# Performance work log

Hardware: AMD Instinct MI355X
Metric: run time of the kernel (lower is better)

Reference implementation:

```python
import jax, jax.numpy as jnp
from jax import lax
import numpy as np

CLASS_NUMBER = 19
REGION_RADIUS = 1
KERNEL = 2 * REGION_RADIUS + 1  # 3
IMAGE_TOPK = 256
EPS = 1e-6


def setup_inputs() -> dict:
    key = jax.random.key(0)
    # softmax-like probabilities over classes
    raw = jax.random.uniform(key, (4, CLASS_NUMBER, 512, 1024), dtype=jnp.float32)
    logit = raw / jnp.sum(raw, axis=1, keepdims=True)
    return {"logit": logit}


def _box_sum(x):
    # kxk box sum with zero padding (SAME for odd kernel == pad=radius)
    return lax.reduce_window(x, jnp.float32(0), lax.add,
                             (1, 1, KERNEL, KERNEL), (1, 1, 1, 1), 'SAME')


def reference(logit):
    B, C, H, W = logit.shape
    logC = jnp.log(jnp.float32(C))

    # region uncertainty: normalized entropy, then avg-pool (count_include_pad)
    entropy = jnp.sum(-logit * jnp.log(logit + EPS), axis=1, keepdims=True) / logC
    region_uncertainty = _box_sum(entropy) / (KERNEL * KERNEL)  # [B,1,H,W]

    # region impurity: argmax -> one-hot -> depthwise box-sum (ones kernel)
    predict = jnp.argmax(logit, axis=1)                       # [B,H,W]
    one_hot = jax.nn.one_hot(predict, C, axis=1, dtype=logit.dtype)  # [B,C,H,W]
    summary = _box_sum(one_hot)                               # [B,C,H,W]
    count = jnp.sum(summary, axis=1, keepdims=True)           # [B,1,H,W]
    dist = summary / count
    region_impurity = jnp.sum(-dist * jnp.log(dist + EPS), axis=1, keepdims=True) / logC

    score = region_uncertainty * region_impurity              # [B,1,H,W]

    # per-image score: sum of top-k region scores
    flat = score.reshape(B, H * W)
    topk_vals, _ = lax.top_k(flat, IMAGE_TOPK)
    image_score = jnp.sum(topk_vals, axis=1)                  # [B]
    return image_score
```

## Files before the change

### kernel.cpp

```cpp
#include <hip/hip_runtime.h>
#include <cstdint>
#include <cstddef>

#define BB 4
#define CC 19
#define HH 512
#define WW 1024
#define HW (HH*WW)
#define HW4 (HW/4)
#define KTOP 256
#define EPSF 1e-6f
#define NB1 4096
#define NB2 8192
#define LSTRIDE 1032
#define LOGC 2.9444389791664403f

#define NSEG 64
#define RPB 8
#define NBLK (BB*NSEG)
#define SEGF 128

__device__ __forceinline__ unsigned int sortable(float x) {
    unsigned int u = __float_as_uint(x);
    return (u & 0x80000000u) ? ~u : (u | 0x80000000u);
}
__device__ __forceinline__ float unsortable(unsigned int K) {
    unsigned int u = (K & 0x80000000u) ? (K & 0x7FFFFFFFu) : ~K;
    return __uint_as_float(u);
}
__device__ __forceinline__ unsigned int agld(const unsigned int* p) {
    return __hip_atomic_load(p, __ATOMIC_RELAXED, __HIP_MEMORY_SCOPE_AGENT);
}
__device__ __forceinline__ void agst(unsigned int* p, unsigned int v) {
    __hip_atomic_store(p, v, __ATOMIC_RELAXED, __HIP_MEMORY_SCOPE_AGENT);
}

struct P1Mem {
    float ent_s[(RPB + 2) * LSTRIDE];
    unsigned char pred_s[(RPB + 2) * LSTRIDE];
    unsigned int lh1[NB1];
};
union UMem { P1Mem p1; unsigned char pad[82000]; };

__global__ __launch_bounds__(1024) void k_init(unsigned int* __restrict__ histb,
                                               float* __restrict__ out) {
    int i = blockIdx.x * 1024 + threadIdx.x;
    if (i < 82180) histb[i] = 0u;
    if (i < BB) out[i] = 0.f;
}

__global__ __launch_bounds__(1024, 4) void k_A(const float* __restrict__ logit,
                                               float* __restrict__ ent,
                                               unsigned char* __restrict__ pred,
                                               float* __restrict__ score,
                                               unsigned int* __restrict__ histb) {
    __shared__ __align__(16) UMem U;
    __shared__ float lgt[48];
    int tid = threadIdx.x;
    int tx = tid & 255;
    int ty = tid >> 8;
    int b = blockIdx.x >> 6;
    int seg = blockIdx.x & (NSEG - 1);
    int r0 = seg * RPB;

    unsigned int* hist1 = histb;
    unsigned int* flags = histb + 81920;

    if (tid < 48) {
        int nvi = tid >> 4, cnt = tid & 15;
        float nv = (nvi == 0) ? 4.f : (nvi == 1) ? 6.f : 9.f;
        lgt[tid] = __logf((float)cnt / nv + EPSF);
    }
    for (int i = tid; i < (RPB + 2) * LSTRIDE; i += 1024) { U.p1.ent_s[i] = 0.f; U.p1.pred_s[i] = 255; }
    for (int i = tid; i < NB1; i += 1024) U.p1.lh1[i] = 0;
    __syncthreads();

    {
        const float4* bb4 = (const float4*)logit + (size_t)b * CC * HW4;
#pragma unroll
        for (int it = 0; it < 2; ++it) {
            int lr = ty + it * 4;
            int q = (r0 + lr) * 256 + tx;
            const float4* basep = bb4 + q;
            float e0 = 0.f, e1 = 0.f, e2 = 0.f, e3 = 0.f;
            float m0 = -1.f, m1 = -1.f, m2 = -1.f, m3 = -1.f;
            int a0 = 0, a1 = 0, a2 = 0, a3 = 0;
#pragma unroll
            for (int c = 0; c < CC; ++c) {
                float4 p = basep[(size_t)c * HW4];
                e0 -= p.x * __logf(p.x + EPSF); if (p.x > m0) { m0 = p.x; a0 = c; }
                e1 -= p.y * __logf(p.y + EPSF); if (p.y > m1) { m1 = p.y; a1 = c; }
                e2 -= p.z * __logf(p.z + EPSF); if (p.z > m2) { m2 = p.z; a2 = c; }
                e3 -= p.w * __logf(p.w + EPSF); if (p.w > m3) { m3 = p.w; a3 = c; }
            }
            *(float4*)&U.p1.ent_s[(lr + 1) * LSTRIDE + 4 + tx * 4] = make_float4(e0, e1, e2, e3);
            unsigned int pw = (unsigned int)a0 | ((unsigned int)a1 << 8) |
                              ((unsigned int)a2 << 16) | ((unsigned int)a3 << 24);
            *(unsigned int*)&U.p1.pred_s[(lr + 1) * LSTRIDE + 4 + tx * 4] = pw;
            if (lr == 0 || lr == RPB - 1) {
                unsigned int* ep = (unsigned int*)ent + (size_t)b * HW + (size_t)(r0 + lr) * WW + tx * 4;
                agst(ep + 0, __float_as_uint(e0));
                agst(ep + 1, __float_as_uint(e1));
                agst(ep + 2, __float_as_uint(e2));
                agst(ep + 3, __float_as_uint(e3));
                agst((unsigned int*)pred + (size_t)b * HW4 + (size_t)(r0 + lr) * 256 + tx, pw);
            }
        }
    }
    __syncthreads();
    if (tid == 0) agst(&flags[blockIdx.x], 1u);
    if (tid == 64 && seg > 0)
        while (agld(&flags[blockIdx.x - 1]) == 0u) __builtin_amdgcn_s_sleep(2);
    if (tid == 128 && seg < NSEG - 1)
        while (agld(&flags[blockIdx.x + 1]) == 0u) __builtin_amdgcn_s_sleep(2);
    __syncthreads();

    if (tid < 512) {
        int top = tid >> 8;
        int c4 = tid & 255;
        int rr = top * (RPB + 1);
        int g = r0 - 1 + top * (RPB + 1);
        if (g >= 0 && g < HH) {
            const unsigned int* eu = (const unsigned int*)ent + (size_t)b * HW + (size_t)g * WW + c4 * 4;
            float4 v;
            v.x = __uint_as_float(agld(eu + 0));
            v.y = __uint_as_float(agld(eu + 1));
            v.z = __uint_as_float(agld(eu + 2));
            v.w = __uint_as_float(agld(eu + 3));
            *(float4*)&U.p1.ent_s[rr * LSTRIDE + 4 + c4 * 4] = v;
            unsigned int pw = agld((const unsigned int*)pred + (size_t)b * HW4 + (size_t)g * 256 + c4);
            *(unsigned int*)&U.p1.pred_s[rr * LSTRIDE + 4 + c4 * 4] = pw;
        }
    }
    __syncthreads();

    float* sbuf = score + (size_t)b * HW;
#pragma unroll
    for (int it = 0; it < 2; ++it) {
        int k = ty + it * 4;
        float r3[3][6];
        int p3[3][6];
#pragma unroll
        for (int rr = 0; rr < 3; ++rr) {
            const float* rowp = &U.p1.ent_s[(k + rr) * LSTRIDE + 4];
            const unsigned char* prow = &U.p1.pred_s[(k + rr) * LSTRIDE + 4];
            float4 m = *(const float4*)&rowp[tx * 4];
            r3[rr][0] = rowp[tx * 4 - 1];
            r3[rr][1] = m.x; r3[rr][2] = m.y; r3[rr][3] = m.z; r3[rr][4] = m.w;
            r3[rr][5] = rowp[tx * 4 + 4];
            uchar4 pm = *(const uchar4*)&prow[tx * 4];
            p3[rr][0] = prow[tx * 4 - 1];
            p3[rr][1] = pm.x; p3[rr][2] = pm.y; p3[rr][3] = pm.z; p3[rr][4] = pm.w;
            p3[rr][5] = prow[tx * 4 + 4];
        }
        int h = r0 + k;
        int hn = (h > 0) + (h < HH - 1) + 1;
        float sv[4];
#pragma unroll
        for (int q = 0; q < 4; ++q) {
            int w = tx * 4 + q;
            float es = 0.f;
#pragma unroll
            for (int i = 0; i < 9; ++i) es += r3[i / 3][q + i % 3];
            int cls[9];
#pragma unroll
            for (int i = 0; i < 9; ++i) cls[i] = p3[i / 3][q + i % 3];
            int nv = hn * ((w > 0) + (w < WW - 1) + 1);
            float inv = 1.f / (float)nv;
            int nvi = (nv == 9) ? 2 : ((nv == 6) ? 1 : 0);
            const float* lg = &lgt[nvi * 16];
            float lsum = 0.f;
#pragma unroll
            for (int i = 0; i < 9; ++i) {
                int cnt = 0;
#pragma unroll
                for (int j = 0; j < 9; ++j) cnt += (cls[j] == cls[i]) ? 1 : 0;
                float lv = lg[cnt];
                lsum += (cls[i] != 255) ? lv : 0.f;
            }
            float imp = -inv * lsum;
            float v = (es * (1.f / (9.f * LOGC))) * (imp * (1.f / LOGC));
            sv[q] = v;
            atomicAdd(&U.p1.lh1[sortable(v) >> 20], 1u);
        }
        *(float4*)&sbuf[(size_t)h * WW + tx * 4] = make_float4(sv[0], sv[1], sv[2], sv[3]);
    }
    __syncthreads();
    {
        unsigned int* hb = hist1 + (size_t)b * NB1;
        for (int i = tid; i < NB1; i += 1024) {
            unsigned int c = U.p1.lh1[i];
            if (c) atomicAdd(&hb[i], c);
        }
    }
}

__device__ __forceinline__ void select4k(const unsigned int* __restrict__ hb,
                                         int rem, int* bin_out, int* rem_out) {
    __shared__ unsigned int cs[256];
    __shared__ unsigned int bs[16];
    __shared__ int s_chunk, s_bin, s_rem;
    int t = threadIdx.x;
    unsigned int s = 0;
#pragma unroll
    for (int i = 0; i < 16; ++i) s += hb[t * 16 + i];
    cs[t] = s;
    __syncthreads();
    for (int d = 1; d < 256; d <<= 1) {
        unsigned int v = (t + d < 256) ? cs[t + d] : 0;
        __syncthreads();
        cs[t] += v;
        __syncthreads();
    }
    unsigned int St = cs[t];
    unsigned int St1 = (t < 255) ? cs[t + 1] : 0;
    if ((int)St >= rem && (t == 255 || (int)St1 < rem)) {
        s_chunk = t; s_rem = rem - (int)St1;
    }
    __syncthreads();
    int chunk = s_chunk, rem2 = s_rem;
    if (t < 16) bs[t] = hb[chunk * 16 + t];
    __syncthreads();
    for (int d = 1; d < 16; d <<= 1) {
        unsigned int v = (t < 16 && t + d < 16) ? bs[t + d] : 0;
        __syncthreads();
        if (t < 16) bs[t] += v;
        __syncthreads();
    }
    if (t < 16) {
        unsigned int Sb = bs[t];
        unsigned int Sb1 = (t < 15) ? bs[t + 1] : 0;
        if ((int)Sb >= rem2 && (t == 15 || (int)Sb1 < rem2)) {
            s_bin = chunk * 16 + t; s_rem = rem2 - (int)Sb1;
        }
    }
    __syncthreads();
    *bin_out = s_bin;
    *rem_out = s_rem;
}

__device__ __forceinline__ void select8k_ag(const unsigned int* __restrict__ hb,
                                            int rem, int* bin_out, int* rem_out) {
    __shared__ unsigned int cs[256];
    __shared__ unsigned int bs[32];
    __shared__ int s_chunk, s_bin, s_rem;
    int t = threadIdx.x;
    unsigned int s = 0;
#pragma unroll 8
    for (int i = 0; i < 32; ++i) s += agld(&hb[t * 32 + i]);
    cs[t] = s;
    __syncthreads();
    for (int d = 1; d < 256; d <<= 1) {
        unsigned int v = (t + d < 256) ? cs[t + d] : 0;
        __syncthreads();
        cs[t] += v;
        __syncthreads();
    }
    unsigned int St = cs[t];
    unsigned int St1 = (t < 255) ? cs[t + 1] : 0;
    if ((int)St >= rem && (t == 255 || (int)St1 < rem)) {
        s_chunk = t; s_rem = rem - (int)St1;
    }
    __syncthreads();
    int chunk = s_chunk, rem2 = s_rem;
    if (t < 32) bs[t] = agld(&hb[chunk * 32 + t]);
    __syncthreads();
    for (int d = 1; d < 32; d <<= 1) {
        unsigned int v = (t < 32 && t + d < 32) ? bs[t + d] : 0;
        __syncthreads();
        if (t < 32) bs[t] += v;
        __syncthreads();
    }
    if (t < 32) {
        unsigned int Sb = bs[t];
        unsigned int Sb1 = (t < 31) ? bs[t + 1] : 0;
        if ((int)Sb >= rem2 && (t == 31 || (int)Sb1 < rem2)) {
            s_bin = chunk * 32 + t; s_rem = rem2 - (int)Sb1;
        }
    }
    __syncthreads();
    *bin_out = s_bin;
    *rem_out = s_rem;
}

__global__ __launch_bounds__(256) void k_B(const float4* __restrict__ score,
                                           const unsigned int* __restrict__ hist1,
                                           unsigned int* __restrict__ hist2,
                                           float* __restrict__ hsum,
                                           unsigned int* __restrict__ done,
                                           float* __restrict__ out) {
    __shared__ unsigned int lh[NB2];
    __shared__ float ls[NB2];
    __shared__ float red[4];
    __shared__ float rs[256];
    __shared__ int islast;
    int b = blockIdx.x >> 7;
    int seg = blockIdx.x & (SEGF - 1);
    int bin1, rem1;
    select4k(hist1 + (size_t)b * NB1, KTOP, &bin1, &rem1);
    unsigned int t1 = (unsigned int)bin1;
    for (int i = threadIdx.x; i < NB2; i += 256) { lh[i] = 0; ls[i] = 0.f; }
    __syncthreads();
    const float4* p = score + ((size_t)b * HW + (size_t)seg * (HW / SEGF)) / 4;
    float sa = 0.f;
    for (int i = threadIdx.x; i < (HW / SEGF) / 4; i += 256) {
        float4 v = p[i];
        float vv[4] = {v.x, v.y, v.z, v.w};
#pragma unroll
        for (int q = 0; q < 4; ++q) {
            unsigned int k = sortable(vv[q]);
            unsigned int cb = k >> 20;
            if (cb > t1) sa += vv[q];
            else if (cb == t1) {
                int sub = (k >> 7) & 0x1FFF;
                atomicAdd(&lh[sub], 1u);
                atomicAdd(&ls[sub], vv[q]);
            }
        }
    }
    __syncthreads();
    {
        unsigned int* hb = hist2 + (size_t)b * NB2;
        float* sb = hsum + (size_t)b * NB2;
        for (int i = threadIdx.x; i < NB2; i += 256) {
            unsigned int c = lh[i];
            if (c) { atomicAdd(&hb[i], c); atomicAdd(&sb[i], ls[i]); }
        }
    }
#pragma unroll
    for (int d = 32; d; d >>= 1) sa += __shfl_down(sa, d);
    if ((threadIdx.x & 63) == 0) red[threadIdx.x >> 6] = sa;
    __syncthreads();
    if (threadIdx.x == 0) {
        float tt = red[0] + red[1] + red[2] + red[3];
        if (tt != 0.f) atomicAdd(&out[b], tt);
    }
    __syncthreads();
    if (threadIdx.x == 0) {
        unsigned int prev = __hip_atomic_fetch_add(&done[b], 1u, __ATOMIC_RELAXED,
                                                   __HIP_MEMORY_SCOPE_AGENT);
        islast = (prev == (unsigned int)(SEGF - 1)) ? 1 : 0;
    }
    __syncthreads();
    if (islast) {
        int bin, rem;
        select8k_ag(hist2 + (size_t)b * NB2, rem1, &bin, &rem);
        const unsigned int* sb = (const unsigned int*)(hsum + (size_t)b * NB2);
        float s = 0.f;
        for (int i = threadIdx.x; i < NB2; i += 256)
            if (i > bin) s += __uint_as_float(agld(&sb[i]));
        rs[threadIdx.x] = s;
        __syncthreads();
        for (int d = 128; d; d >>= 1) {
            if (threadIdx.x < d) rs[threadIdx.x] += rs[threadIdx.x + d];
            __syncthreads();
        }
        if (threadIdx.x == 0) {
            unsigned int K = (t1 << 20) | ((unsigned int)bin << 7);
            atomicAdd(&out[b], rs[0] + unsortable(K) * (float)rem);
        }
    }
}

extern "C" void kernel_launch(void* const* d_in, const int* in_sizes, int n_in,
                              void* d_out, int out_size, void* d_ws, size_t ws_size,
                              hipStream_t stream) {
    const float* logit = (const float*)d_in[0];
    float* out = (float*)d_out;
    char* ws = (char*)d_ws;

    float*         ent   = (float*)(ws);
    unsigned char* pred  = (unsigned char*)(ws + 8388608);
    float*         score = (float*)(ws + 10485760);
    unsigned int*  histb = (unsigned int*)(ws + 18874368);
    unsigned int*  hist1 = histb;
    unsigned int*  hist2 = histb + 16384;
    float*         hsum  = (float*)(histb + 49152);
    unsigned int*  done  = histb + 82176;

    k_init<<<81, 1024, 0, stream>>>(histb, out);
    k_A<<<NBLK, 1024, 0, stream>>>(logit, ent, pred, score, histb);
    k_B<<<BB * SEGF, 256, 0, stream>>>((const float4*)score, hist1, hist2, hsum, done, out);
}
```

Before: 289.9 us.

## Recompute halo rows per block instead of exchanging them via global flags

```diff
diff --git a/kernel.cpp b/kernel.cpp
--- a/kernel.cpp
+++ b/kernel.cpp
@@ -18,6 +18,7 @@
 #define NSEG 64
 #define RPB 8
 #define NBLK (BB*NSEG)
+#define TPB 1024
 #define SEGF 128
 
 __device__ __forceinline__ unsigned int sortable(float x) {
@@ -31,31 +32,26 @@
 __device__ __forceinline__ unsigned int agld(const unsigned int* p) {
     return __hip_atomic_load(p, __ATOMIC_RELAXED, __HIP_MEMORY_SCOPE_AGENT);
 }
-__device__ __forceinline__ void agst(unsigned int* p, unsigned int v) {
-    __hip_atomic_store(p, v, __ATOMIC_RELAXED, __HIP_MEMORY_SCOPE_AGENT);
-}
-
-struct P1Mem {
+
+__global__ __launch_bounds__(1024) void k_init(unsigned int* __restrict__ histb,
+                                               float* __restrict__ out) {
+    int i = blockIdx.x * 1024 + threadIdx.x;
+    if (i < 81924) histb[i] = 0u;
+    if (i < BB) out[i] = 0.f;
+}
+
+struct AMem {
     float ent_s[(RPB + 2) * LSTRIDE];
     unsigned char pred_s[(RPB + 2) * LSTRIDE];
     unsigned int lh1[NB1];
 };
-union UMem { P1Mem p1; unsigned char pad[82000]; };
-
-__global__ __launch_bounds__(1024) void k_init(unsigned int* __restrict__ histb,
-                                               float* __restrict__ out) {
-    int i = blockIdx.x * 1024 + threadIdx.x;
-    if (i < 82180) histb[i] = 0u;
-    if (i < BB) out[i] = 0.f;
-}
 
 __global__ __launch_bounds__(1024, 4) void k_A(const float* __restrict__ logit,
-                                               float* __restrict__ ent,
-                                               unsigned char* __restrict__ pred,
                                                float* __restrict__ score,
-                                               unsigned int* __restrict__ histb) {
-    __shared__ __align__(16) UMem U;
+                                               unsigned int* __restrict__ hist1) {
+    __shared__ __align__(16) AMem U;
     __shared__ float lgt[48];
+
     int tid = threadIdx.x;
     int tx = tid & 255;
     int ty = tid >> 8;
@@ -63,25 +59,23 @@
     int seg = blockIdx.x & (NSEG - 1);
     int r0 = seg * RPB;
 
-    unsigned int* hist1 = histb;
-    unsigned int* flags = histb + 81920;
-
     if (tid < 48) {
         int nvi = tid >> 4, cnt = tid & 15;
         float nv = (nvi == 0) ? 4.f : (nvi == 1) ? 6.f : 9.f;
         lgt[tid] = __logf((float)cnt / nv + EPSF);
     }
-    for (int i = tid; i < (RPB + 2) * LSTRIDE; i += 1024) { U.p1.ent_s[i] = 0.f; U.p1.pred_s[i] = 255; }
-    for (int i = tid; i < NB1; i += 1024) U.p1.lh1[i] = 0;
+    for (int i = tid; i < (RPB + 2) * LSTRIDE; i += TPB) { U.ent_s[i] = 0.f; U.pred_s[i] = 255; }
+    for (int i = tid; i < NB1; i += TPB) U.lh1[i] = 0;
     __syncthreads();
 
     {
         const float4* bb4 = (const float4*)logit + (size_t)b * CC * HW4;
-#pragma unroll
-        for (int it = 0; it < 2; ++it) {
-            int lr = ty + it * 4;
-            int q = (r0 + lr) * 256 + tx;
-            const float4* basep = bb4 + q;
+        for (int t = tid; t < (RPB + 2) * 256; t += TPB) {
+            int lr = t >> 8;
+            int cq = t & 255;
+            int g = r0 - 1 + lr;
+            if (g < 0 || g >= HH) continue;
+            const float4* basep = bb4 + (size_t)g * 256 + cq;
             float e0 = 0.f, e1 = 0.f, e2 = 0.f, e3 = 0.f;
             float m0 = -1.f, m1 = -1.f, m2 = -1.f, m3 = -1.f;
             int a0 = 0, a1 = 0, a2 = 0, a3 = 0;
@@ -93,43 +87,10 @@
                 e2 -= p.z * __logf(p.z + EPSF); if (p.z > m2) { m2 = p.z; a2 = c; }
                 e3 -= p.w * __logf(p.w + EPSF); if (p.w > m3) { m3 = p.w; a3 = c; }
             }
-            *(float4*)&U.p1.ent_s[(lr + 1) * LSTRIDE + 4 + tx * 4] = make_float4(e0, e1, e2, e3);
+            *(float4*)&U.ent_s[lr * LSTRIDE + 4 + cq * 4] = make_float4(e0, e1, e2, e3);
             unsigned int pw = (unsigned int)a0 | ((unsigned int)a1 << 8) |
                               ((unsigned int)a2 << 16) | ((unsigned int)a3 << 24);
-            *(unsigned int*)&U.p1.pred_s[(lr + 1) * LSTRIDE + 4 + tx * 4] = pw;
-            if (lr == 0 || lr == RPB - 1) {
-                unsigned int* ep = (unsigned int*)ent + (size_t)b * HW + (size_t)(r0 + lr) * WW + tx * 4;
-                agst(ep + 0, __float_as_uint(e0));
-                agst(ep + 1, __float_as_uint(e1));
-                agst(ep + 2, __float_as_uint(e2));
-                agst(ep + 3, __float_as_uint(e3));
-                agst((unsigned int*)pred + (size_t)b * HW4 + (size_t)(r0 + lr) * 256 + tx, pw);
-            }
-        }
-    }
-    __syncthreads();
-    if (tid == 0) agst(&flags[blockIdx.x], 1u);
-    if (tid == 64 && seg > 0)
-        while (agld(&flags[blockIdx.x - 1]) == 0u) __builtin_amdgcn_s_sleep(2);
-    if (tid == 128 && seg < NSEG - 1)
-        while (agld(&flags[blockIdx.x + 1]) == 0u) __builtin_amdgcn_s_sleep(2);
-    __syncthreads();
-
-    if (tid < 512) {
-        int top = tid >> 8;
-        int c4 = tid & 255;
-        int rr = top * (RPB + 1);
-        int g = r0 - 1 + top * (RPB + 1);
-        if (g >= 0 && g < HH) {
-            const unsigned int* eu = (const unsigned int*)ent + (size_t)b * HW + (size_t)g * WW + c4 * 4;
-            float4 v;
-            v.x = __uint_as_float(agld(eu + 0));
-            v.y = __uint_as_float(agld(eu + 1));
-            v.z = __uint_as_float(agld(eu + 2));
-            v.w = __uint_as_float(agld(eu + 3));
-            *(float4*)&U.p1.ent_s[rr * LSTRIDE + 4 + c4 * 4] = v;
-            unsigned int pw = agld((const unsigned int*)pred + (size_t)b * HW4 + (size_t)g * 256 + c4);
-            *(unsigned int*)&U.p1.pred_s[rr * LSTRIDE + 4 + c4 * 4] = pw;
+            *(unsigned int*)&U.pred_s[lr * LSTRIDE + 4 + cq * 4] = pw;
         }
     }
     __syncthreads();
@@ -142,8 +103,8 @@
         int p3[3][6];
 #pragma unroll
         for (int rr = 0; rr < 3; ++rr) {
-            const float* rowp = &U.p1.ent_s[(k + rr) * LSTRIDE + 4];
-            const unsigned char* prow = &U.p1.pred_s[(k + rr) * LSTRIDE + 4];
+            const float* rowp = &U.ent_s[(k + rr) * LSTRIDE + 4];
+            const unsigned char* prow = &U.pred_s[(k + rr) * LSTRIDE + 4];
             float4 m = *(const float4*)&rowp[tx * 4];
             r3[rr][0] = rowp[tx * 4 - 1];
             r3[rr][1] = m.x; r3[rr][2] = m.y; r3[rr][3] = m.z; r3[rr][4] = m.w;
@@ -181,15 +142,15 @@
             float imp = -inv * lsum;
             float v = (es * (1.f / (9.f * LOGC))) * (imp * (1.f / LOGC));
             sv[q] = v;
-            atomicAdd(&U.p1.lh1[sortable(v) >> 20], 1u);
+            atomicAdd(&U.lh1[sortable(v) >> 20], 1u);
         }
         *(float4*)&sbuf[(size_t)h * WW + tx * 4] = make_float4(sv[0], sv[1], sv[2], sv[3]);
     }
     __syncthreads();
     {
         unsigned int* hb = hist1 + (size_t)b * NB1;
-        for (int i = tid; i < NB1; i += 1024) {
-            unsigned int c = U.p1.lh1[i];
+        for (int i = tid; i < NB1; i += TPB) {
+            unsigned int c = U.lh1[i];
             if (c) atomicAdd(&hb[i], c);
         }
     }
@@ -369,16 +330,14 @@
     float* out = (float*)d_out;
     char* ws = (char*)d_ws;
 
-    float*         ent   = (float*)(ws);
-    unsigned char* pred  = (unsigned char*)(ws + 8388608);
-    float*         score = (float*)(ws + 10485760);
-    unsigned int*  histb = (unsigned int*)(ws + 18874368);
+    float*         score = (float*)(ws);
+    unsigned int*  histb = (unsigned int*)(ws + 8388608);
     unsigned int*  hist1 = histb;
     unsigned int*  hist2 = histb + 16384;
     float*         hsum  = (float*)(histb + 49152);
-    unsigned int*  done  = histb + 82176;
+    unsigned int*  done  = histb + 81920;
 
     k_init<<<81, 1024, 0, stream>>>(histb, out);
-    k_A<<<NBLK, 1024, 0, stream>>>(logit, ent, pred, score, histb);
+    k_A<<<NBLK, TPB, 0, stream>>>(logit, score, hist1);
     k_B<<<BB * SEGF, 256, 0, stream>>>((const float4*)score, hist1, hist2, hsum, done, out);
 }
```

Measured after the change: 285.5 us. No clear change (-1.5%).
